# Kernel optimization log

Hardware: AMD Instinct MI355X
Metric: run time of the kernel (lower is better)

Reference implementation:

```python
import jax, jax.numpy as jnp
import numpy as np

B, T, EMB, HEAD = 8, 2048, 1024, 1024

def setup_inputs() -> dict:
    key = jax.random.key(0)
    k1, k2, k3, k4 = jax.random.split(key, 4)
    s = 1.0 / np.sqrt(EMB)
    return {
        "x": jax.random.normal(k1, (B, T, EMB), dtype=jnp.float32),
        "Wq": jax.random.normal(k2, (HEAD, EMB), dtype=jnp.float32) * s,
        "Wk": jax.random.normal(k3, (HEAD, EMB), dtype=jnp.float32) * s,
        "Wv": jax.random.normal(k4, (HEAD, EMB), dtype=jnp.float32) * s,
    }

def reference(x, Wq, Wk, Wv):
    # Bias-free projections; torch Linear weight is [out, in] -> contract on last dim.
    q = jnp.einsum('btc,hc->bth', x, Wq)  # [B,T,HEAD]
    k = jnp.einsum('btc,hc->bth', x, Wk)
    v = jnp.einsum('btc,hc->bth', x, Wv)
    C = x.shape[-1]
    scale = jnp.asarray(C, x.dtype) ** -0.5  # NOTE: scales by emb dim C, as in source
    wei = jnp.einsum('bth,bsh->bts', q, k) * scale  # [B,T,T]
    Tn = x.shape[1]
    causal = jnp.tril(jnp.ones((Tn, Tn), dtype=bool))
    wei = jnp.where(causal, wei, -jnp.inf)
    wei = jax.nn.softmax(wei, axis=-1)
    # dropout omitted (eval mode / deterministic reference)
    out = jnp.einsum('bts,bsh->bth', wei, v)  # [B,T,HEAD]
    return out
```

## Files before the change

kernel.cpp:

```cpp
#include <hip/hip_runtime.h>

typedef unsigned short u16;
typedef short short8 __attribute__((ext_vector_type(8)));
typedef float f32x4 __attribute__((ext_vector_type(4)));

#define WS_K_OFF    33554432ULL
#define WS_PTRI     67108864ULL
#define WS_PART     104857600ULL
#define WS_NEED     105447424ULL

__device__ __forceinline__ u16 f2bf(float f) {
    union { float f; unsigned u; } c; c.f = f;
    unsigned r = c.u + 0x7fffu + ((c.u >> 16) & 1u);
    return (u16)(r >> 16);
}
__device__ __forceinline__ float bf2f(u16 h) {
    union { unsigned u; float f; } c; c.u = ((unsigned)h) << 16; return c.f;
}
__device__ __forceinline__ void gll16(const u16* g, u16* l) {
    __builtin_amdgcn_global_load_lds(
        (const __attribute__((address_space(1))) void*)g,
        (__attribute__((address_space(3))) void*)l, 16, 0, 0);
}

template<int AMODE>
__device__ __forceinline__ void gemm_pipe(
    const u16* __restrict__ A, int lda,
    const u16* __restrict__ B, int ldb,
    int m0, int n0, int nk, u16* lds, f32x4 acc[8][4])
{
    const int tid  = threadIdx.x;
    const int lane = tid & 63;
    const int w    = tid >> 6;
    const int wm   = w >> 2, wn = w & 3;
    const int kg   = lane >> 4, l15 = lane & 15;
    const int r0   = w * 32 + (lane >> 2);
    const int s0   = (lane & 3) ^ ((r0 >> 1) & 3);

    const int ldA = AMODE ? 256 : lda;
    const u16* Ar0 = A + (size_t)(m0 + r0) * ldA + s0 * 8;
    const u16* Ar1 = Ar0 + 16 * ldA;
    const u16* Br0 = B + (size_t)(n0 + r0) * ldb + s0 * 8;
    const u16* Br1 = Br0 + 16 * ldb;

    auto aoff = [&](int t) -> int {
        return AMODE ? ((t >> 3) * 65536 + (t & 7) * 32) : t * 32;
    };
    auto STAGE = [&](int t) {
        const int ao = aoff(t), bo = t * 32, buf = (t & 3) * 16384;
        u16* dA = lds + buf + w * 1024;
        u16* dB = lds + buf + 8192 + w * 1024;
        gll16(Ar0 + ao, dA);
        gll16(Ar1 + ao, dA + 512);
        gll16(Br0 + bo, dB);
        gll16(Br1 + bo, dB + 512);
    };
    auto LDA8 = [&](short8* fa, int t) {
        const u16* h = lds + (t & 3) * 16384 + wm * 4096;
        #pragma unroll
        for (int mt = 0; mt < 8; ++mt) {
            const int row = mt * 16 + l15;
            fa[mt] = *reinterpret_cast<const short8*>(
                h + row * 32 + ((kg ^ ((row >> 1) & 3)) << 3));
        }
    };
    auto LDB4 = [&](short8* fb, int t) {
        const u16* h = lds + (t & 3) * 16384 + 8192 + wn * 2048;
        #pragma unroll
        for (int nt = 0; nt < 4; ++nt) {
            const int row = nt * 16 + l15;
            fb[nt] = *reinterpret_cast<const short8*>(
                h + row * 32 + ((kg ^ ((row >> 1) & 3)) << 3));
        }
    };
    auto MFMA32 = [&](short8* fa, short8* fb) {
        __builtin_amdgcn_s_setprio(1);
        #pragma unroll
        for (int mt = 0; mt < 8; ++mt)
            #pragma unroll
            for (int nt = 0; nt < 4; ++nt)
                acc[mt][nt] = __builtin_amdgcn_mfma_f32_16x16x32_bf16(
                    fa[mt], fb[nt], acc[mt][nt], 0, 0, 0);
        __builtin_amdgcn_s_setprio(0);
    };

    STAGE(0); STAGE(1); STAGE(2);
    asm volatile("s_waitcnt vmcnt(4)" ::: "memory");
    __builtin_amdgcn_s_barrier();

    short8 faA[8], faB[8], fb[4];
    LDA8(faA, 0);

    for (int t = 0; t < nk; t += 2) {
        LDB4(fb, t);
        LDA8(faB, t + 1);
        if (t + 3 < nk) STAGE(t + 3);
        MFMA32(faA, fb);
        if (t + 3 < nk) asm volatile("s_waitcnt vmcnt(4)" ::: "memory");
        else            asm volatile("s_waitcnt vmcnt(0)" ::: "memory");
        __builtin_amdgcn_s_barrier();

        LDB4(fb, t + 1);
        if (t + 2 < nk) LDA8(faA, t + 2);
        if (t + 4 < nk) STAGE(t + 4);
        MFMA32(faB, fb);
        if (t + 4 < nk) asm volatile("s_waitcnt vmcnt(4)" ::: "memory");
        else            asm volatile("s_waitcnt vmcnt(0)" ::: "memory");
        __builtin_amdgcn_s_barrier();
    }
}

__global__ __launch_bounds__(256) void cvt_bf16(
    const float* __restrict__ x,
    const float* __restrict__ Wq,
    const float* __restrict__ Wk,
    const float* __restrict__ Wv,
    u16* __restrict__ dst)
{
    const size_t e = ((size_t)blockIdx.x * 256 + threadIdx.x) * 8;
    const float* src;
    if (e < (size_t)16777216) {
        src = x + e;
    } else {
        size_t j = e - 16777216;
        int z = (int)(j >> 20);
        const float* Wz = (z == 0) ? Wq : (z == 1) ? Wk : Wv;
        src = Wz + (j & 1048575);
    }
    float4 a = *reinterpret_cast<const float4*>(src);
    float4 b = *reinterpret_cast<const float4*>(src + 4);
    short8 v;
    v[0] = (short)f2bf(a.x); v[1] = (short)f2bf(a.y);
    v[2] = (short)f2bf(a.z); v[3] = (short)f2bf(a.w);
    v[4] = (short)f2bf(b.x); v[5] = (short)f2bf(b.y);
    v[6] = (short)f2bf(b.z); v[7] = (short)f2bf(b.w);
    *reinterpret_cast<short8*>(dst + e) = v;
}

__global__ __launch_bounds__(512, 2) void qkv_pipe(
    const u16* __restrict__ xb, const u16* __restrict__ Wb,
    u16* __restrict__ Qo, u16* __restrict__ Ko, u16* __restrict__ VTo, int zbase)
{
    __shared__ u16 L[65536];
    const int tid = threadIdx.x, lane = tid & 63, w = tid >> 6;
    const int wm = w >> 2, wn = w & 3, kg = lane >> 4, l15 = lane & 15;
    const int m0 = blockIdx.x * 256, n0 = blockIdx.y * 256;
    const int z = blockIdx.z + zbase;

    const f32x4 z4 = {0.f, 0.f, 0.f, 0.f};
    f32x4 acc[8][4];
    #pragma unroll
    for (int i = 0; i < 8; ++i)
        #pragma unroll
        for (int j = 0; j < 4; ++j) acc[i][j] = z4;

    gemm_pipe<0>(xb, 1024, Wb + (size_t)z * 1048576, 1024, m0, n0, 32, L, acc);

    if (z < 2) {
        u16* O = (z == 0) ? Qo : Ko;
        #pragma unroll
        for (int mt = 0; mt < 8; ++mt) {
            const int row0 = m0 + wm * 128 + mt * 16 + kg * 4;
            #pragma unroll
            for (int nt = 0; nt < 4; ++nt) {
                const int col = n0 + wn * 64 + nt * 16 + l15;
                #pragma unroll
                for (int r = 0; r < 4; ++r)
                    O[(size_t)(row0 + r) * 1024 + col] = f2bf(acc[mt][nt][r]);
            }
        }
    } else {
        #pragma unroll
        for (int mt = 0; mt < 8; ++mt) {
            const int row0 = m0 + wm * 128 + mt * 16 + kg * 4;
            #pragma unroll
            for (int nt = 0; nt < 4; ++nt) {
                const int col = n0 + wn * 64 + nt * 16 + l15;
                #pragma unroll
                for (int r = 0; r < 4; ++r) {
                    const int rr = row0 + r;
                    VTo[((size_t)(rr >> 11) * 1024 + col) * 2048 + (rr & 2047)] = f2bf(acc[mt][nt][r]);
                }
            }
        }
    }
}

__global__ __launch_bounds__(512, 2) void sp128(
    const u16* __restrict__ Q, const u16* __restrict__ K,
    u16* __restrict__ Ptri, float* __restrict__ part)
{
    __shared__ u16 L[49152];
    int jj = blockIdx.x;
    const int b = jj / 72;
    int r = jj - b * 72;
    int qb = 0;
    while (r >= 2 * qb + 2) { r -= 2 * qb + 2; ++qb; }
    const int kb = r;

    const int tid = threadIdx.x, lane = tid & 63, w = tid >> 6;
    const int wm = w >> 1, wn = w & 1, kg = lane >> 4, l15 = lane & 15;

    const int rA = w * 32 + (lane >> 2);
    const int sA = (lane & 3) ^ ((rA >> 1) & 3);
    const int rB = w * 16 + (lane >> 2);
    const int sB = (lane & 3) ^ ((rB >> 1) & 3);
    const u16* Ar0 = Q + (size_t)(b * 2048 + qb * 256 + rA) * 1024 + sA * 8;
    const u16* Ar1 = Ar0 + 16 * 1024;
    const u16* Br0 = K + (size_t)(b * 2048 + kb * 128 + rB) * 1024 + sB * 8;

    const f32x4 z4 = {0.f, 0.f, 0.f, 0.f};
    f32x4 acc[4][4];
    #pragma unroll
    for (int a_ = 0; a_ < 4; ++a_)
        #pragma unroll
        for (int j = 0; j < 4; ++j) acc[a_][j] = z4;

    auto STAGE = [&](int t) {
        const int buf = (t & 3) * 12288;
        gll16(Ar0 + t * 32, L + buf + w * 1024);
        gll16(Ar1 + t * 32, L + buf + w * 1024 + 512);
        gll16(Br0 + t * 32, L + buf + 8192 + w * 512);
    };
    auto LDA4 = [&](short8* fa, int t) {
        const u16* h = L + (t & 3) * 12288;
        #pragma unroll
        for (int mt = 0; mt < 4; ++mt) {
            const int row = wm * 64 + mt * 16 + l15;
            fa[mt] = *reinterpret_cast<const short8*>(
                h + row * 32 + ((kg ^ ((row >> 1) & 3)) << 3));
        }
    };
    auto LDB4 = [&](short8* fb, int t) {
        const u16* h = L + (t & 3) * 12288 + 8192;
        #pragma unroll
        for (int nt = 0; nt < 4; ++nt) {
            const int row = wn * 64 + nt * 16 + l15;
            fb[nt] = *reinterpret_cast<const short8*>(
                h + row * 32 + ((kg ^ ((row >> 1) & 3)) << 3));
        }
    };
    auto MFMA16 = [&](short8* fa, short8* fb) {
        __builtin_amdgcn_s_setprio(1);
        #pragma unroll
        for (int mt = 0; mt < 4; ++mt)
            #pragma unroll
            for (int nt = 0; nt < 4; ++nt)
                acc[mt][nt] = __builtin_amdgcn_mfma_f32_16x16x32_bf16(
                    fa[mt], fb[nt], acc[mt][nt], 0, 0, 0);
        __builtin_amdgcn_s_setprio(0);
    };

    const int nk = 32;
    STAGE(0); STAGE(1); STAGE(2);
    asm volatile("s_waitcnt vmcnt(3)" ::: "memory");
    __builtin_amdgcn_s_barrier();

    short8 faA[4], faB[4], fb[4];
    LDA4(faA, 0);
    for (int t = 0; t < nk; t += 2) {
        LDB4(fb, t);
        LDA4(faB, t + 1);
        if (t + 3 < nk) STAGE(t + 3);
        MFMA16(faA, fb);
        if (t + 3 < nk) asm volatile("s_waitcnt vmcnt(3)" ::: "memory");
        else            asm volatile("s_waitcnt vmcnt(0)" ::: "memory");
        __builtin_amdgcn_s_barrier();

        LDB4(fb, t + 1);
        if (t + 2 < nk) LDA4(faA, t + 2);
        if (t + 4 < nk) STAGE(t + 4);
        MFMA16(faB, fb);
        if (t + 4 < nk) asm volatile("s_waitcnt vmcnt(3)" ::: "memory");
        else            asm volatile("s_waitcnt vmcnt(0)" ::: "memory");
        __builtin_amdgcn_s_barrier();
    }

    u16* Pt = Ptri + ((size_t)b * 36 + (qb * (qb + 1)) / 2 + (kb >> 1)) * 65536
                   + (kb & 1) * 128;
    float* psum = (float*)L;
    #pragma unroll
    for (int mt = 0; mt < 4; ++mt) {
        #pragma unroll
        for (int rr = 0; rr < 4; ++rr) {
            const int lt = wm * 64 + mt * 16 + kg * 4 + rr;
            const int gt = qb * 256 + lt;
            float ps = 0.f;
            #pragma unroll
            for (int nt = 0; nt < 4; ++nt) {
                const int lcol = wn * 64 + nt * 16 + l15;
                const int gs = kb * 128 + lcol;
                const float p = (gs <= gt) ? __expf(acc[mt][nt][rr] * 0.03125f) : 0.f;
                ps += p;
                Pt[(size_t)lt * 256 + lcol] = f2bf(p);
            }
            #pragma unroll
            for (int d = 1; d < 16; d <<= 1) ps += __shfl_xor(ps, d, 64);
            if (l15 == 0) psum[lt * 2 + wn] = ps;
        }
    }
    __syncthreads();
    if (tid < 256) {
        const float s = psum[tid * 2] + psum[tid * 2 + 1];
        part[(size_t)b * 18432 + (qb * qb + qb) * 256 + tid * (2 * qb + 2) + kb] = s;
    }
}

__global__ __launch_bounds__(512, 2) void sp_old(
    const u16* __restrict__ Q, const u16* __restrict__ K, u16* __restrict__ P)
{
    const int qb = blockIdx.x, kb = blockIdx.y, b = blockIdx.z;
    if (kb > qb) return;
    __shared__ u16 L[65536];
    const int tid = threadIdx.x, lane = tid & 63, w = tid >> 6;
    const int wm = w >> 2, wn = w & 3, kg = lane >> 4, l15 = lane & 15;

    const f32x4 z4 = {0.f, 0.f, 0.f, 0.f};
    f32x4 acc[8][4];
    #pragma unroll
    for (int i = 0; i < 8; ++i)
        #pragma unroll
        for (int j = 0; j < 4; ++j) acc[i][j] = z4;

    gemm_pipe<0>(Q, 1024, K, 1024, b * 2048 + qb * 256, b * 2048 + kb * 256, 32, L, acc);

    u16* Pb = P + (size_t)b * 2048 * 2048;
    #pragma unroll
    for (int mt = 0; mt < 8; ++mt) {
        const int trow0 = qb * 256 + wm * 128 + mt * 16 + kg * 4;
        #pragma unroll
        for (int nt = 0; nt < 4; ++nt) {
            const int scol = kb * 256 + wn * 64 + nt * 16 + l15;
            #pragma unroll
            for (int r = 0; r < 4; ++r) {
                const int trow = trow0 + r;
                const float p = (scol <= trow) ? __expf(acc[mt][nt][r] * 0.03125f) : 0.f;
                Pb[(size_t)trow * 2048 + scol] = f2bf(p);
            }
        }
    }
}

__global__ __launch_bounds__(512, 2) void pv128(
    const u16* __restrict__ Ptri, const u16* __restrict__ VT,
    const float* __restrict__ part, float* __restrict__ out)
{
    __shared__ u16 L[49152];
    const int i = blockIdx.x;
    const int q  = 7 - (i >> 6);
    const int b  = (i >> 3) & 7;
    const int nb = i & 7;
    const int nk = (q + 1) * 8;

    const int tid = threadIdx.x, lane = tid & 63, w = tid >> 6;
    const int wm = w >> 1, wn = w & 1, kg = lane >> 4, l15 = lane & 15;

    const u16* A = Ptri + ((size_t)b * 36 + (q * (q + 1)) / 2) * 65536;
    const u16* B = VT + ((size_t)b * 1024 + nb * 128) * 2048;

    const int rA = w * 32 + (lane >> 2);
    const int sA = (lane & 3) ^ ((rA >> 1) & 3);
    const int rB = w * 16 + (lane >> 2);
    const int sB = (lane & 3) ^ ((rB >> 1) & 3);
    const u16* Ar0 = A + (size_t)rA * 256 + sA * 8;
    const u16* Ar1 = Ar0 + 16 * 256;
    const u16* Br0 = B + (size_t)rB * 2048 + sB * 8;

    const f32x4 z4 = {0.f, 0.f, 0.f, 0.f};
    f32x4 acc[4][4];
    #pragma unroll
    for (int a_ = 0; a_ < 4; ++a_)
        #pragma unroll
        for (int j = 0; j < 4; ++j) acc[a_][j] = z4;

    auto aoff = [&](int t) -> int { return (t >> 3) * 65536 + (t & 7) * 32; };
    auto STAGE = [&](int t) {
        const int buf = (t & 3) * 12288;
        gll16(Ar0 + aoff(t), L + buf + w * 1024);
        gll16(Ar1 + aoff(t), L + buf + w * 1024 + 512);
        gll16(Br0 + t * 32, L + buf + 8192 + w * 512);
    };
    auto LDA4 = [&](short8* fa, int t) {
        const u16* h = L + (t & 3) * 12288;
        #pragma unroll
        for (int mt = 0; mt < 4; ++mt) {
            const int row = wm * 64 + mt * 16 + l15;
            fa[mt] = *reinterpret_cast<const short8*>(
                h + row * 32 + ((kg ^ ((row >> 1) & 3)) << 3));
        }
    };
    auto LDB4 = [&](short8* fb, int t) {
        const u16* h = L + (t & 3) * 12288 + 8192;
        #pragma unroll
        for (int nt = 0; nt < 4; ++nt) {
            const int row = wn * 64 + nt * 16 + l15;
            fb[nt] = *reinterpret_cast<const short8*>(
                h + row * 32 + ((kg ^ ((row >> 1) & 3)) << 3));
        }
    };
    auto MFMA16 = [&](short8* fa, short8* fb) {
        __builtin_amdgcn_s_setprio(1);
        #pragma unroll
        for (int mt = 0; mt < 4; ++mt)
            #pragma unroll
            for (int nt = 0; nt < 4; ++nt)
                acc[mt][nt] = __builtin_amdgcn_mfma_f32_16x16x32_bf16(
                    fa[mt], fb[nt], acc[mt][nt], 0, 0, 0);
        __builtin_amdgcn_s_setprio(0);
    };

    STAGE(0); STAGE(1); STAGE(2);
    asm volatile("s_waitcnt vmcnt(3)" ::: "memory");
    __builtin_amdgcn_s_barrier();

    short8 faA[4], faB[4], fb[4];
    LDA4(faA, 0);
    for (int t = 0; t < nk; t += 2) {
        LDB4(fb, t);
        LDA4(faB, t + 1);
        if (t + 3 < nk) STAGE(t + 3);
        MFMA16(faA, fb);
        if (t + 3 < nk) asm volatile("s_waitcnt vmcnt(3)" ::: "memory");
        else            asm volatile("s_waitcnt vmcnt(0)" ::: "memory");
        __builtin_amdgcn_s_barrier();

        LDB4(fb, t + 1);
        if (t + 2 < nk) LDA4(faA, t + 2);
        if (t + 4 < nk) STAGE(t + 4);
        MFMA16(faB, fb);
        if (t + 4 < nk) asm volatile("s_waitcnt vmcnt(3)" ::: "memory");
        else            asm volatile("s_waitcnt vmcnt(0)" ::: "memory");
        __builtin_amdgcn_s_barrier();
    }

    float* Lf = (float*)L;
    if (tid < 256) {
        const int nkb = 2 * q + 2;
        const float* pp = part + (size_t)b * 18432 + (q * q + q) * 256 + tid * nkb;
        float s = 0.f;
        for (int kb = 0; kb < nkb; ++kb) s += pp[kb];
        Lf[tid] = 1.f / s;
    }
    __syncthreads();

    #pragma unroll
    for (int mt = 0; mt < 4; ++mt) {
        const int lt0 = wm * 64 + mt * 16 + kg * 4;
        const size_t grow0 = (size_t)b * 2048 + q * 256 + lt0;
        float rs[4];
        #pragma unroll
        for (int r = 0; r < 4; ++r) rs[r] = Lf[lt0 + r];
        #pragma unroll
        for (int nt = 0; nt < 4; ++nt) {
            const int col = nb * 128 + wn * 64 + nt * 16 + l15;
            #pragma unroll
            for (int r = 0; r < 4; ++r)
                out[(grow0 + r) * 1024 + col] = acc[mt][nt][r] * rs[r];
        }
    }
}

__global__ __launch_bounds__(512, 2) void pv_old(
    const u16* __restrict__ P, const u16* __restrict__ VT, float* __restrict__ Of)
{
    const int b = blockIdx.x >> 3, qblk = blockIdx.x & 7;
    const int nb = blockIdx.y;
    const int nk = (qblk + 1) * 8;
    __shared__ u16 L[65536];
    const int tid = threadIdx.x, lane = tid & 63, w = tid >> 6;
    const int wm = w >> 2, wn = w & 3, kg = lane >> 4, l15 = lane & 15;

    const f32x4 z4 = {0.f, 0.f, 0.f, 0.f};
    f32x4 acc[8][4];
    #pragma unroll
    for (int i = 0; i < 8; ++i)
        #pragma unroll
        for (int j = 0; j < 4; ++j) acc[i][j] = z4;

    gemm_pipe<0>(P + (size_t)b * 2048 * 2048, 2048,
                 VT + (size_t)b * 1024 * 2048, 2048,
                 qblk * 256, nb * 256, nk, L, acc);

    #pragma unroll
    for (int mt = 0; mt < 8; ++mt) {
        const int trow0 = qblk * 256 + wm * 128 + mt * 16 + kg * 4;
        #pragma unroll
        for (int nt = 0; nt < 4; ++nt) {
            const int col = nb * 256 + wn * 64 + nt * 16 + l15;
            #pragma unroll
            for (int r = 0; r < 4; ++r)
                Of[((size_t)b * 2048 + trow0 + r) * 1024 + col] = acc[mt][nt][r];
        }
    }
}

__global__ __launch_bounds__(256) void finalize(
    const u16* __restrict__ P, const float* __restrict__ Of, float* __restrict__ out)
{
    const int row = blockIdx.x;
    const int tid = threadIdx.x;
    const int b = row >> 11, t = row & 2047;
    const int len = ((t >> 8) + 1) * 256;
    const u16* prow = P + ((size_t)b * 2048 + t) * 2048;

    float s = 0.f;
    const int i = tid * 8;
    if (i < len) {
        short8 v = *reinterpret_cast<const short8*>(prow + i);
        #pragma unroll
        for (int j = 0; j < 8; ++j) s += bf2f((u16)v[j]);
    }
    #pragma unroll
    for (int d = 1; d < 64; d <<= 1) s += __shfl_xor(s, d, 64);

    __shared__ float red[4];
    if ((tid & 63) == 0) red[tid >> 6] = s;
    __syncthreads();
    const float rinv = 1.f / (red[0] + red[1] + red[2] + red[3]);

    const size_t o = (size_t)row * 1024 + tid * 4;
    f32x4 v = *reinterpret_cast<const f32x4*>(Of + o);
    v[0] *= rinv; v[1] *= rinv; v[2] *= rinv; v[3] *= rinv;
    *reinterpret_cast<f32x4*>(out + o) = v;
}

extern "C" void kernel_launch(void* const* d_in, const int* in_sizes, int n_in,
                              void* d_out, int out_size, void* d_ws, size_t ws_size,
                              hipStream_t stream) {
    const float* x  = (const float*)d_in[0];
    const float* Wq = (const float*)d_in[1];
    const float* Wk = (const float*)d_in[2];
    const float* Wv = (const float*)d_in[3];

    u16* xb = (u16*)d_out;
    u16* Wb = xb + (size_t)16777216;

    cvt_bf16<<<dim3(9728), 256, 0, stream>>>(x, Wq, Wk, Wv, xb);

    if (ws_size >= WS_NEED) {
        u16*   Qb   = (u16*)d_ws;
        u16*   Kb   = (u16*)((char*)d_ws + WS_K_OFF);
        u16*   Pt   = (u16*)((char*)d_ws + WS_PTRI);
        float* part = (float*)((char*)d_ws + WS_PART);
        u16*   VTb  = Qb;

        qkv_pipe<<<dim3(64, 4, 2), 512, 0, stream>>>(xb, Wb, Qb, Kb, Qb, 0);
        sp128<<<dim3(576), 512, 0, stream>>>(Qb, Kb, Pt, part);
        qkv_pipe<<<dim3(64, 4, 1), 512, 0, stream>>>(xb, Wb, Qb, Kb, VTb, 2);
        pv128<<<dim3(512), 512, 0, stream>>>(Pt, VTb, part, (float*)d_out);
    } else {
        u16* Qb  = (u16*)d_ws;
        u16* Kb  = Qb + (size_t)16384 * 1024;
        u16* VTb = Kb + (size_t)16384 * 1024;
        float* Of = (float*)d_ws;
        u16* Pb = (u16*)d_out;

        qkv_pipe<<<dim3(64, 4, 3), 512, 0, stream>>>(xb, Wb, Qb, Kb, VTb, 0);
        sp_old<<<dim3(8, 8, 8), 512, 0, stream>>>(Qb, Kb, Pb);
        pv_old<<<dim3(64, 4), 512, 0, stream>>>(Pb, VTb, Of);
        finalize<<<dim3(16384), 256, 0, stream>>>(Pb, Of, (float*)d_out);
    }
}
```

Measured before the change: 261.5 us.

## Shrink GEMM pipeline to triple-buffered LDS and interleave PV block scheduling

Factors the shared bf16 MFMA main loop of the score and PV kernels into a common helper. The helper uses three LDS stages prefetched two ahead instead of four stages three ahead, with single-buffered fragments, cutting LDS per block from 96KB to 72KB. The launch bound is raised to request more resident blocks per CU. The PV kernel's block index now alternates heavy and light causal query blocks to balance load. The risk is less latency hiding from the shallower prefetch and register pressure under the tighter bound.

```diff
diff --git a/kernel.cpp b/kernel.cpp
--- a/kernel.cpp
+++ b/kernel.cpp
@@ -186,11 +186,79 @@
     }
 }
 
-__global__ __launch_bounds__(512, 2) void sp128(
+template<int AMODE>
+__device__ __forceinline__ void gemm_tri128(
+    const u16* __restrict__ A, int lda,
+    const u16* __restrict__ B, int ldb, int nk, u16* L, f32x4 acc[4][4])
+{
+    const int tid = threadIdx.x, lane = tid & 63, w = tid >> 6;
+    const int wm = w >> 1, wn = w & 1, kg = lane >> 4, l15 = lane & 15;
+
+    const int rA = w * 32 + (lane >> 2);
+    const int sA = (lane & 3) ^ ((rA >> 1) & 3);
+    const int rB = w * 16 + (lane >> 2);
+    const int sB = (lane & 3) ^ ((rB >> 1) & 3);
+    const int ldA = AMODE ? 256 : lda;
+    const u16* Ar0 = A + (size_t)rA * ldA + sA * 8;
+    const u16* Ar1 = Ar0 + 16 * ldA;
+    const u16* Br0 = B + (size_t)rB * ldb + sB * 8;
+
+    auto aoff = [&](int t) -> int {
+        return AMODE ? ((t >> 3) * 65536 + (t & 7) * 32) : t * 32;
+    };
+    auto STAGE = [&](int t) {
+        u16* d = L + (t % 3) * 12288;
+        gll16(Ar0 + aoff(t), d + w * 1024);
+        gll16(Ar1 + aoff(t), d + w * 1024 + 512);
+        gll16(Br0 + t * 32,  d + 8192 + w * 512);
+    };
+    auto LDA4 = [&](short8* fa, int t) {
+        const u16* h = L + (t % 3) * 12288;
+        #pragma unroll
+        for (int mt = 0; mt < 4; ++mt) {
+            const int row = wm * 64 + mt * 16 + l15;
+            fa[mt] = *reinterpret_cast<const short8*>(
+                h + row * 32 + ((kg ^ ((row >> 1) & 3)) << 3));
+        }
+    };
+    auto LDB4 = [&](short8* fb, int t) {
+        const u16* h = L + (t % 3) * 12288 + 8192;
+        #pragma unroll
+        for (int nt = 0; nt < 4; ++nt) {
+            const int row = wn * 64 + nt * 16 + l15;
+            fb[nt] = *reinterpret_cast<const short8*>(
+                h + row * 32 + ((kg ^ ((row >> 1) & 3)) << 3));
+        }
+    };
+
+    STAGE(0); STAGE(1);
+    asm volatile("s_waitcnt vmcnt(3)" ::: "memory");
+    __builtin_amdgcn_s_barrier();
+
+    short8 fa[4], fb[4];
+    for (int t = 0; t < nk; ++t) {
+        LDA4(fa, t);
+        LDB4(fb, t);
+        if (t + 2 < nk) STAGE(t + 2);
+        __builtin_amdgcn_s_setprio(1);
+        #pragma unroll
+        for (int mt = 0; mt < 4; ++mt)
+            #pragma unroll
+            for (int nt = 0; nt < 4; ++nt)
+                acc[mt][nt] = __builtin_amdgcn_mfma_f32_16x16x32_bf16(
+                    fa[mt], fb[nt], acc[mt][nt], 0, 0, 0);
+        __builtin_amdgcn_s_setprio(0);
+        if (t + 2 < nk) asm volatile("s_waitcnt vmcnt(3)" ::: "memory");
+        else            asm volatile("s_waitcnt vmcnt(0)" ::: "memory");
+        __builtin_amdgcn_s_barrier();
+    }
+}
+
+__global__ __launch_bounds__(512, 4) void sp128(
     const u16* __restrict__ Q, const u16* __restrict__ K,
     u16* __restrict__ Ptri, float* __restrict__ part)
 {
-    __shared__ u16 L[49152];
+    __shared__ u16 L[36864];
     int jj = blockIdx.x;
     const int b = jj / 72;
     int r = jj - b * 72;
@@ -201,14 +269,6 @@
     const int tid = threadIdx.x, lane = tid & 63, w = tid >> 6;
     const int wm = w >> 1, wn = w & 1, kg = lane >> 4, l15 = lane & 15;
 
-    const int rA = w * 32 + (lane >> 2);
-    const int sA = (lane & 3) ^ ((rA >> 1) & 3);
-    const int rB = w * 16 + (lane >> 2);
-    const int sB = (lane & 3) ^ ((rB >> 1) & 3);
-    const u16* Ar0 = Q + (size_t)(b * 2048 + qb * 256 + rA) * 1024 + sA * 8;
-    const u16* Ar1 = Ar0 + 16 * 1024;
-    const u16* Br0 = K + (size_t)(b * 2048 + kb * 128 + rB) * 1024 + sB * 8;
-
     const f32x4 z4 = {0.f, 0.f, 0.f, 0.f};
     f32x4 acc[4][4];
     #pragma unroll
@@ -216,65 +276,9 @@
         #pragma unroll
         for (int j = 0; j < 4; ++j) acc[a_][j] = z4;
 
-    auto STAGE = [&](int t) {
-        const int buf = (t & 3) * 12288;
-        gll16(Ar0 + t * 32, L + buf + w * 1024);
-        gll16(Ar1 + t * 32, L + buf + w * 1024 + 512);
-        gll16(Br0 + t * 32, L + buf + 8192 + w * 512);
-    };
-    auto LDA4 = [&](short8* fa, int t) {
-        const u16* h = L + (t & 3) * 12288;
-        #pragma unroll
-        for (int mt = 0; mt < 4; ++mt) {
-            const int row = wm * 64 + mt * 16 + l15;
-            fa[mt] = *reinterpret_cast<const short8*>(
-                h + row * 32 + ((kg ^ ((row >> 1) & 3)) << 3));
-        }
-    };
-    auto LDB4 = [&](short8* fb, int t) {
-        const u16* h = L + (t & 3) * 12288 + 8192;
-        #pragma unroll
-        for (int nt = 0; nt < 4; ++nt) {
-            const int row = wn * 64 + nt * 16 + l15;
-            fb[nt] = *reinterpret_cast<const short8*>(
-                h + row * 32 + ((kg ^ ((row >> 1) & 3)) << 3));
-        }
-    };
-    auto MFMA16 = [&](short8* fa, short8* fb) {
-        __builtin_amdgcn_s_setprio(1);
-        #pragma unroll
-        for (int mt = 0; mt < 4; ++mt)
-            #pragma unroll
-            for (int nt = 0; nt < 4; ++nt)
-                acc[mt][nt] = __builtin_amdgcn_mfma_f32_16x16x32_bf16(
-                    fa[mt], fb[nt], acc[mt][nt], 0, 0, 0);
-        __builtin_amdgcn_s_setprio(0);
-    };
-
-    const int nk = 32;
-    STAGE(0); STAGE(1); STAGE(2);
-    asm volatile("s_waitcnt vmcnt(3)" ::: "memory");
-    __builtin_amdgcn_s_barrier();
-
-    short8 faA[4], faB[4], fb[4];
-    LDA4(faA, 0);
-    for (int t = 0; t < nk; t += 2) {
-        LDB4(fb, t);
-        LDA4(faB, t + 1);
-        if (t + 3 < nk) STAGE(t + 3);
-        MFMA16(faA, fb);
-        if (t + 3 < nk) asm volatile("s_waitcnt vmcnt(3)" ::: "memory");
-        else            asm volatile("s_waitcnt vmcnt(0)" ::: "memory");
-        __builtin_amdgcn_s_barrier();
-
-        LDB4(fb, t + 1);
-        if (t + 2 < nk) LDA4(faA, t + 2);
-        if (t + 4 < nk) STAGE(t + 4);
-        MFMA16(faB, fb);
-        if (t + 4 < nk) asm volatile("s_waitcnt vmcnt(3)" ::: "memory");
-        else            asm volatile("s_waitcnt vmcnt(0)" ::: "memory");
-        __builtin_amdgcn_s_barrier();
-    }
+    gemm_tri128<0>(Q + (size_t)(b * 2048 + qb * 256) * 1024, 1024,
+                   K + (size_t)(b * 2048 + kb * 128) * 1024, 1024,
+                   32, L, acc);
 
     u16* Pt = Ptri + ((size_t)b * 36 + (qb * (qb + 1)) / 2 + (kb >> 1)) * 65536
                    + (kb & 1) * 128;
@@ -341,105 +345,41 @@
     }
 }
 
-__global__ __launch_bounds__(512, 2) void pv128(
+__global__ __launch_bounds__(512, 4) void pv128(
     const u16* __restrict__ Ptri, const u16* __restrict__ VT,
     const float* __restrict__ part, float* __restrict__ out)
 {
-    __shared__ u16 L[49152];
+    __shared__ u16 L[36864];
     const int i = blockIdx.x;
-    const int q  = 7 - (i >> 6);
-    const int b  = (i >> 3) & 7;
-    const int nb = i & 7;
+    const int c = i >> 7;
+    const int j = (i >> 1) & 63;
+    const int s = i & 1;
+    const int q  = s ? c : 7 - c;
+    const int b  = j >> 3;
+    const int nb = j & 7;
     const int nk = (q + 1) * 8;
 
     const int tid = threadIdx.x, lane = tid & 63, w = tid >> 6;
     const int wm = w >> 1, wn = w & 1, kg = lane >> 4, l15 = lane & 15;
 
-    const u16* A = Ptri + ((size_t)b * 36 + (q * (q + 1)) / 2) * 65536;
-    const u16* B = VT + ((size_t)b * 1024 + nb * 128) * 2048;
-
-    const int rA = w * 32 + (lane >> 2);
-    const int sA = (lane & 3) ^ ((rA >> 1) & 3);
-    const int rB = w * 16 + (lane >> 2);
-    const int sB = (lane & 3) ^ ((rB >> 1) & 3);
-    const u16* Ar0 = A + (size_t)rA * 256 + sA * 8;
-    const u16* Ar1 = Ar0 + 16 * 256;
-    const u16* Br0 = B + (size_t)rB * 2048 + sB * 8;
-
     const f32x4 z4 = {0.f, 0.f, 0.f, 0.f};
     f32x4 acc[4][4];
     #pragma unroll
     for (int a_ = 0; a_ < 4; ++a_)
         #pragma unroll
-        for (int j = 0; j < 4; ++j) acc[a_][j] = z4;
-
-    auto aoff = [&](int t) -> int { return (t >> 3) * 65536 + (t & 7) * 32; };
-    auto STAGE = [&](int t) {
-        const int buf = (t & 3) * 12288;
-        gll16(Ar0 + aoff(t), L + buf + w * 1024);
-        gll16(Ar1 + aoff(t), L + buf + w * 1024 + 512);
-        gll16(Br0 + t * 32, L + buf + 8192 + w * 512);
-    };
-    auto LDA4 = [&](short8* fa, int t) {
-        const u16* h = L + (t & 3) * 12288;
-        #pragma unroll
-        for (int mt = 0; mt < 4; ++mt) {
-            const int row = wm * 64 + mt * 16 + l15;
-            fa[mt] = *reinterpret_cast<const short8*>(
-                h + row * 32 + ((kg ^ ((row >> 1) & 3)) << 3));
-        }
-    };
-    auto LDB4 = [&](short8* fb, int t) {
-        const u16* h = L + (t & 3) * 12288 + 8192;
-        #pragma unroll
-        for (int nt = 0; nt < 4; ++nt) {
-            const int row = wn * 64 + nt * 16 + l15;
-            fb[nt] = *reinterpret_cast<const short8*>(
-                h + row * 32 + ((kg ^ ((row >> 1) & 3)) << 3));
-        }
-    };
-    auto MFMA16 = [&](short8* fa, short8* fb) {
-        __builtin_amdgcn_s_setprio(1);
-        #pragma unroll
-        for (int mt = 0; mt < 4; ++mt)
-            #pragma unroll
-            for (int nt = 0; nt < 4; ++nt)
-                acc[mt][nt] = __builtin_amdgcn_mfma_f32_16x16x32_bf16(
-                    fa[mt], fb[nt], acc[mt][nt], 0, 0, 0);
-        __builtin_amdgcn_s_setprio(0);
-    };
-
-    STAGE(0); STAGE(1); STAGE(2);
-    asm volatile("s_waitcnt vmcnt(3)" ::: "memory");
-    __builtin_amdgcn_s_barrier();
-
-    short8 faA[4], faB[4], fb[4];
-    LDA4(faA, 0);
-    for (int t = 0; t < nk; t += 2) {
-        LDB4(fb, t);
-        LDA4(faB, t + 1);
-        if (t + 3 < nk) STAGE(t + 3);
-        MFMA16(faA, fb);
-        if (t + 3 < nk) asm volatile("s_waitcnt vmcnt(3)" ::: "memory");
-        else            asm volatile("s_waitcnt vmcnt(0)" ::: "memory");
-        __builtin_amdgcn_s_barrier();
-
-        LDB4(fb, t + 1);
-        if (t + 2 < nk) LDA4(faA, t + 2);
-        if (t + 4 < nk) STAGE(t + 4);
-        MFMA16(faB, fb);
-        if (t + 4 < nk) asm volatile("s_waitcnt vmcnt(3)" ::: "memory");
-        else            asm volatile("s_waitcnt vmcnt(0)" ::: "memory");
-        __builtin_amdgcn_s_barrier();
-    }
+        for (int jx = 0; jx < 4; ++jx) acc[a_][jx] = z4;
+
+    gemm_tri128<1>(Ptri + ((size_t)b * 36 + (q * (q + 1)) / 2) * 65536, 256,
+                   VT + ((size_t)b * 1024 + nb * 128) * 2048, 2048,
+                   nk, L, acc);
 
     float* Lf = (float*)L;
     if (tid < 256) {
         const int nkb = 2 * q + 2;
         const float* pp = part + (size_t)b * 18432 + (q * q + q) * 256 + tid * nkb;
-        float s = 0.f;
-        for (int kb = 0; kb < nkb; ++kb) s += pp[kb];
-        Lf[tid] = 1.f / s;
+        float sum = 0.f;
+        for (int kb = 0; kb < nkb; ++kb) sum += pp[kb];
+        Lf[tid] = 1.f / sum;
     }
     __syncthreads();
 
```

Result: no change. 260.4 us (-0.4%).
